# Kernel optimization log

Hardware: AMD Instinct MI355X
Metric: run time of the kernel (lower is better)

The kernel has to match this reference:

```python
import jax, jax.numpy as jnp
import numpy as np

K_NEIGHBORS = 8  # sparse_reads


def setup_inputs() -> dict:
    key = jax.random.key(0)
    k1, k2, k3, k4 = jax.random.split(key, 4)
    b, m, w, r, d_in = 32, 65536, 32, 4, 256
    xi = jax.random.normal(k1, (b, d_in), jnp.float32)
    sparse = jax.random.normal(k2, (b, m, w), jnp.float32)
    W_rk = jax.random.normal(k3, (r * w, d_in), jnp.float32) * 0.05  # read_keys_transform weight
    b_rk = jax.random.normal(k4, (r * w,), jnp.float32) * 0.01       # read_keys_transform bias
    return {"xi": xi, "sparse": sparse, "W_rk": W_rk, "b_rk": b_rk}


def reference(xi, sparse, W_rk, b_rk):
    b = xi.shape[0]
    m, w = sparse.shape[1], sparse.shape[2]
    r = W_rk.shape[0] // w
    # read keys: Linear(input_size, r*w) -> [b, r, w]
    read_keys = (xi @ W_rk.T + b_rk).reshape(b, r, w)
    # exact kNN replacing FLANN: squared L2 distances [b, r, m]
    d2 = (
        jnp.sum(read_keys * read_keys, -1)[..., None]
        - 2.0 * jnp.einsum('brw,bmw->brm', read_keys, sparse)
        + jnp.sum(sparse * sparse, -1)[:, None, :]
    )
    neg_d, idx = jax.lax.top_k(-d2, K_NEIGHBORS)  # K smallest distances
    dist = -neg_d                                  # [b, r, K]
    # gather the K nearest memory rows per (batch, head): [b, r, K, w]
    vecs = sparse[jnp.arange(b)[:, None, None], idx]
    # distances normalized by their max (per key), as in `distances / max(distances)`
    read_weights = dist / jnp.max(dist, -1, keepdims=True)
    # torch code stacks per-key over batch then over keys -> [r, b, K, w]
    read_vectors = jnp.transpose(vecs, (1, 0, 2, 3))
    read_weights = jnp.transpose(read_weights, (1, 0, 2))  # [r, b, K]
    return read_vectors, read_weights
```

## Files before the change

kernel.cpp:

```cpp
#include <hip/hip_runtime.h>

constexpr int Bb = 32;
constexpr int Mm = 65536;
constexpr int Ww = 32;
constexpr int Rr = 4;
constexpr int Dd = 256;
constexpr int Kk = 8;

constexpr int NB_A = 64;
constexpr int TPB_A = 256;
constexpr int ROWS_PER_BLOCK = Mm / NB_A;
constexpr int TILE_ROWS = 128;
constexpr int TILES = ROWS_PER_BLOCK / TILE_ROWS;
constexpr int NBUF = 3;
constexpr int GRP_F4 = 65;
constexpr int TILE_F4 = (TILE_ROWS / 8) * GRP_F4;
constexpr int CPL = NB_A * Kk / 64;

__device__ __forceinline__ void glds16(const float4* src, float4* dst_lds) {
  __builtin_amdgcn_global_load_lds(
      (const __attribute__((address_space(1))) void*)src,
      (__attribute__((address_space(3))) void*)dst_lds, 16, 0, 0);
}

__global__ __launch_bounds__(128) void rk_kernel(
    const float* __restrict__ xi, const float* __restrict__ Wrk,
    const float* __restrict__ brk, float* __restrict__ rk,
    float* __restrict__ rknorm) {
  const int b = blockIdx.x;
  const int tid = threadIdx.x;
  __shared__ float xs[Dd];
  __shared__ float rks[Rr * Ww];
  #pragma unroll
  for (int i = 0; i < Dd; i += 128) xs[i + tid] = xi[b * Dd + i + tid];
  __syncthreads();
  float acc = brk[tid];
  const float4* wr = reinterpret_cast<const float4*>(Wrk + (size_t)tid * Dd);
  #pragma unroll 4
  for (int i = 0; i < Dd / 4; ++i) {
    float4 wv = wr[i];
    acc = fmaf(wv.x, xs[4 * i + 0], acc);
    acc = fmaf(wv.y, xs[4 * i + 1], acc);
    acc = fmaf(wv.z, xs[4 * i + 2], acc);
    acc = fmaf(wv.w, xs[4 * i + 3], acc);
  }
  rk[b * Rr * Ww + tid] = acc;
  rks[tid] = acc;
  __syncthreads();
  if (tid < Rr) {
    float s = 0.f;
    #pragma unroll
    for (int j = 0; j < Ww; ++j) s = fmaf(rks[tid * Ww + j], rks[tid * Ww + j], s);
    rknorm[b * Rr + tid] = s;
  }
}

__global__ __launch_bounds__(TPB_A, 2) void topk_partial(
    const float* __restrict__ sparse, const float* __restrict__ rk,
    const float* __restrict__ rknorm, float* __restrict__ cand_d,
    int* __restrict__ cand_i) {
  const int b = blockIdx.y;
  const int tid = threadIdx.x;
  const int lane = tid & 63;
  const int wid = tid >> 6;
  const float INF = __builtin_inff();

  __shared__ float4 rk4[Rr][8];
  __shared__ float rkn_s[Rr];
  __shared__ float4 tile[NBUF][TILE_F4];

  if (tid < Rr * Ww) reinterpret_cast<float*>(rk4)[tid] = rk[b * Rr * Ww + tid];
  if (tid < Rr) rkn_s[tid] = rknorm[b * Rr + tid];
  __syncthreads();

  float rkn[Rr];
  #pragma unroll
  for (int r = 0; r < Rr; ++r) rkn[r] = rkn_s[r];

  const int rowBlk = blockIdx.x * ROWS_PER_BLOCK;
  const float4* sb4 =
      reinterpret_cast<const float4*>(sparse) + (size_t)b * Mm * 8;

  const int rowL = wid * 32 + (lane >> 1);
  const int hsel = (tid & 1) * 4;
  const int rbase = (rowL >> 3) * GRP_F4 + (rowL & 7) * 8;

  float d8[Rr][TILES];

  auto STAGE = [&](int buf, int t) {
    const float4* g0 = sb4 + (size_t)(rowBlk + t * TILE_ROWS + wid * 32) * 8;
    #pragma unroll
    for (int i = 0; i < 4; ++i)
      glds16(g0 + i * 64 + lane, &tile[buf][(wid * 4 + i) * GRP_F4]);
  };

  STAGE(0, 0);
  STAGE(1, 1);
  #pragma unroll
  for (int t = 0; t < TILES; ++t) {
    if (t + 2 < TILES) {
      asm volatile("s_waitcnt lgkmcnt(0)" ::: "memory");
      STAGE((t + 2) % NBUF, t + 2);
      asm volatile("s_waitcnt vmcnt(8)" ::: "memory");
    } else if (t + 1 < TILES) {
      asm volatile("s_waitcnt vmcnt(4)" ::: "memory");
    } else {
      asm volatile("s_waitcnt vmcnt(0)" ::: "memory");
    }
    const float4* tb = &tile[t % NBUF][rbase];
    float a0 = 0.f, a1 = 0.f, a2 = 0.f, a3 = 0.f, ss = 0.f;
    #pragma unroll
    for (int j = 0; j < 4; ++j) {
      float4 v = tb[hsel + j];
      float4 k0 = rk4[0][hsel + j];
      float4 k1 = rk4[1][hsel + j];
      float4 k2 = rk4[2][hsel + j];
      float4 k3 = rk4[3][hsel + j];
      a0 = fmaf(k0.x, v.x, a0); a0 = fmaf(k0.y, v.y, a0);
      a0 = fmaf(k0.z, v.z, a0); a0 = fmaf(k0.w, v.w, a0);
      a1 = fmaf(k1.x, v.x, a1); a1 = fmaf(k1.y, v.y, a1);
      a1 = fmaf(k1.z, v.z, a1); a1 = fmaf(k1.w, v.w, a1);
      a2 = fmaf(k2.x, v.x, a2); a2 = fmaf(k2.y, v.y, a2);
      a2 = fmaf(k2.z, v.z, a2); a2 = fmaf(k2.w, v.w, a2);
      a3 = fmaf(k3.x, v.x, a3); a3 = fmaf(k3.y, v.y, a3);
      a3 = fmaf(k3.z, v.z, a3); a3 = fmaf(k3.w, v.w, a3);
      ss = fmaf(v.x, v.x, ss); ss = fmaf(v.y, v.y, ss);
      ss = fmaf(v.z, v.z, ss); ss = fmaf(v.w, v.w, ss);
    }
    float p0 = fmaf(-2.f, a0, ss);
    float p1 = fmaf(-2.f, a1, ss);
    float p2 = fmaf(-2.f, a2, ss);
    float p3 = fmaf(-2.f, a3, ss);
    p0 += __shfl_xor(p0, 1);
    p1 += __shfl_xor(p1, 1);
    p2 += __shfl_xor(p2, 1);
    p3 += __shfl_xor(p3, 1);
    d8[0][t] = p0 + rkn[0];
    d8[1][t] = p1 + rkn[1];
    d8[2][t] = p2 + rkn[2];
    d8[3][t] = p3 + rkn[3];
  }

  __syncthreads();
  float* dmp = reinterpret_cast<float*>(&tile[0][0]);
  if ((tid & 1) == 0) {
    const int e = tid >> 1;
    #pragma unroll
    for (int r = 0; r < Rr; ++r) {
      float4* p = reinterpret_cast<float4*>(&dmp[(r * 128 + e) * 8]);
      p[0] = make_float4(d8[r][0], d8[r][1], d8[r][2], d8[r][3]);
      p[1] = make_float4(d8[r][4], d8[r][5], d8[r][6], d8[r][7]);
    }
  }
  __syncthreads();

  {
    const int r = wid;
    const int e0 = 2 * lane;
    float v[2][TILES];
    #pragma unroll
    for (int q = 0; q < 2; ++q) {
      const float4* p =
          reinterpret_cast<const float4*>(&dmp[(r * 128 + e0 + q) * 8]);
      float4 lo = p[0], hi = p[1];
      v[q][0] = lo.x; v[q][1] = lo.y; v[q][2] = lo.z; v[q][3] = lo.w;
      v[q][4] = hi.x; v[q][5] = hi.y; v[q][6] = hi.z; v[q][7] = hi.w;
    }
    const int base = rowBlk + e0;
    size_t o = ((size_t)(b * Rr + r) * NB_A + blockIdx.x) * Kk;
    #pragma unroll
    for (int k = 0; k < Kk; ++k) {
      float lv = v[0][0];
      int lrow = base;
      #pragma unroll
      for (int q = 0; q < 2; ++q)
        #pragma unroll
        for (int s = 0; s < TILES; ++s) {
          if (q == 0 && s == 0) continue;
          int row = base + q + s * TILE_ROWS;
          if (v[q][s] < lv || (v[q][s] == lv && row < lrow)) {
            lv = v[q][s]; lrow = row;
          }
        }
      float bv = lv;
      int bi = lrow;
      #pragma unroll
      for (int off = 32; off; off >>= 1) {
        float ov = __shfl_xor(bv, off);
        int oi = __shfl_xor(bi, off);
        if (ov < bv || (ov == bv && oi < bi)) { bv = ov; bi = oi; }
      }
      if (lane == 0) { cand_d[o + k] = bv; cand_i[o + k] = bi; }
      #pragma unroll
      for (int q = 0; q < 2; ++q)
        #pragma unroll
        for (int s = 0; s < TILES; ++s) {
          bool clr = (v[q][s] == bv) && (base + q + s * TILE_ROWS == bi);
          v[q][s] = clr ? INF : v[q][s];
        }
    }
  }
}

__global__ __launch_bounds__(64) void topk_final(
    const float* __restrict__ sparse, const float* __restrict__ cand_d,
    const int* __restrict__ cand_i, float* __restrict__ out) {
  const int br = blockIdx.x;
  const int b = br >> 2;
  const int r = br & 3;
  const int lane = threadIdx.x;
  const float INF = __builtin_inff();

  float ld[CPL];
  int li[CPL];
  const float* cd = cand_d + (size_t)br * (NB_A * Kk);
  const int* ci = cand_i + (size_t)br * (NB_A * Kk);
  #pragma unroll
  for (int t = 0; t < CPL; ++t) {
    ld[t] = cd[t * 64 + lane];
    li[t] = ci[t * 64 + lane];
  }
  #pragma unroll
  for (int i = 0; i < CPL - 1; ++i)
    #pragma unroll
    for (int j = 0; j < CPL - 1 - i; ++j)
      if (ld[j + 1] < ld[j] || (ld[j + 1] == ld[j] && li[j + 1] < li[j])) {
        float td = ld[j]; ld[j] = ld[j + 1]; ld[j + 1] = td;
        int ti = li[j]; li[j] = li[j + 1]; li[j + 1] = ti;
      }

  __shared__ float s_td[Kk];
  __shared__ int s_ti[Kk];
  #pragma unroll
  for (int k = 0; k < Kk; ++k) {
    float v = ld[0];
    int id = li[0];
    #pragma unroll
    for (int off = 32; off; off >>= 1) {
      float ov = __shfl_xor(v, off);
      int oi = __shfl_xor(id, off);
      if (ov < v || (ov == v && oi < id)) { v = ov; id = oi; }
    }
    if (lane == 0) { s_td[k] = v; s_ti[k] = id; }
    if (li[0] == id) {
      #pragma unroll
      for (int j = 0; j < CPL - 1; ++j) { ld[j] = ld[j + 1]; li[j] = li[j + 1]; }
      ld[CPL - 1] = INF;
      li[CPL - 1] = -1;
    }
  }
  __syncthreads();

  const float dmax = s_td[Kk - 1];
  if (lane < Kk)
    out[(size_t)Rr * Bb * Kk * Ww + ((size_t)r * Bb + b) * Kk + lane] =
        s_td[lane] / dmax;

  const float* sbase = sparse + (size_t)b * Mm * Ww;
  #pragma unroll
  for (int t = 0; t < (Kk * Ww) / 64; ++t) {
    int e = t * 64 + lane;
    int k = e >> 5;
    int j = e & 31;
    out[(((size_t)r * Bb + b) * Kk + k) * Ww + j] =
        sbase[(size_t)s_ti[k] * Ww + j];
  }
}

extern "C" void kernel_launch(void* const* d_in, const int* in_sizes, int n_in,
                              void* d_out, int out_size, void* d_ws,
                              size_t ws_size, hipStream_t stream) {
  const float* xi = (const float*)d_in[0];
  const float* sparse = (const float*)d_in[1];
  const float* Wrk = (const float*)d_in[2];
  const float* brk = (const float*)d_in[3];
  float* out = (float*)d_out;

  char* ws = (char*)d_ws;
  float* rk = (float*)ws;
  float* rknorm = (float*)(ws + 16384);
  float* cand_d = (float*)(ws + 16896);
  int* cand_i = (int*)(ws + 16896 + 262144);

  rk_kernel<<<Bb, 128, 0, stream>>>(xi, Wrk, brk, rk, rknorm);
  dim3 gridA(NB_A, Bb);
  topk_partial<<<gridA, TPB_A, 0, stream>>>(sparse, rk, rknorm, cand_d, cand_i);
  topk_final<<<Bb * Rr, 64, 0, stream>>>(sparse, cand_d, cand_i, out);
}
```

Measured before the change: 91.84 us.

## Replace LDS-staged async tile loads with register double-buffered direct global loads

```diff
diff --git a/kernel.cpp b/kernel.cpp
--- a/kernel.cpp
+++ b/kernel.cpp
@@ -12,16 +12,7 @@
 constexpr int ROWS_PER_BLOCK = Mm / NB_A;
 constexpr int TILE_ROWS = 128;
 constexpr int TILES = ROWS_PER_BLOCK / TILE_ROWS;
-constexpr int NBUF = 3;
-constexpr int GRP_F4 = 65;
-constexpr int TILE_F4 = (TILE_ROWS / 8) * GRP_F4;
 constexpr int CPL = NB_A * Kk / 64;
-
-__device__ __forceinline__ void glds16(const float4* src, float4* dst_lds) {
-  __builtin_amdgcn_global_load_lds(
-      (const __attribute__((address_space(1))) void*)src,
-      (__attribute__((address_space(3))) void*)dst_lds, 16, 0, 0);
-}
 
 __global__ __launch_bounds__(128) void rk_kernel(
     const float* __restrict__ xi, const float* __restrict__ Wrk,
@@ -67,7 +58,7 @@
 
   __shared__ float4 rk4[Rr][8];
   __shared__ float rkn_s[Rr];
-  __shared__ float4 tile[NBUF][TILE_F4];
+  __shared__ float dmp[Rr * TILE_ROWS * TILES];
 
   if (tid < Rr * Ww) reinterpret_cast<float*>(rk4)[tid] = rk[b * Rr * Ww + tid];
   if (tid < Rr) rkn_s[tid] = rknorm[b * Rr + tid];
@@ -78,40 +69,30 @@
   for (int r = 0; r < Rr; ++r) rkn[r] = rkn_s[r];
 
   const int rowBlk = blockIdx.x * ROWS_PER_BLOCK;
-  const float4* sb4 =
-      reinterpret_cast<const float4*>(sparse) + (size_t)b * Mm * 8;
-
   const int rowL = wid * 32 + (lane >> 1);
   const int hsel = (tid & 1) * 4;
-  const int rbase = (rowL >> 3) * GRP_F4 + (rowL & 7) * 8;
+
+  const float4* rp = reinterpret_cast<const float4*>(sparse) +
+                     (size_t)b * Mm * 8 + (size_t)(rowBlk + rowL) * 8 + hsel;
 
   float d8[Rr][TILES];
 
-  auto STAGE = [&](int buf, int t) {
-    const float4* g0 = sb4 + (size_t)(rowBlk + t * TILE_ROWS + wid * 32) * 8;
-    #pragma unroll
-    for (int i = 0; i < 4; ++i)
-      glds16(g0 + i * 64 + lane, &tile[buf][(wid * 4 + i) * GRP_F4]);
-  };
-
-  STAGE(0, 0);
-  STAGE(1, 1);
+  float4 La0, La1, La2, La3, Lb0, Lb1, Lb2, Lb3;
+  La0 = rp[0]; La1 = rp[1]; La2 = rp[2]; La3 = rp[3];
   #pragma unroll
   for (int t = 0; t < TILES; ++t) {
-    if (t + 2 < TILES) {
-      asm volatile("s_waitcnt lgkmcnt(0)" ::: "memory");
-      STAGE((t + 2) % NBUF, t + 2);
-      asm volatile("s_waitcnt vmcnt(8)" ::: "memory");
-    } else if (t + 1 < TILES) {
-      asm volatile("s_waitcnt vmcnt(4)" ::: "memory");
-    } else {
-      asm volatile("s_waitcnt vmcnt(0)" ::: "memory");
-    }
-    const float4* tb = &tile[t % NBUF][rbase];
+    const float4* np = rp + (size_t)(t + 1) * TILE_ROWS * 8;
+    float4 v0, v1, v2, v3;
+    if (t & 1) { v0 = Lb0; v1 = Lb1; v2 = Lb2; v3 = Lb3; }
+    else       { v0 = La0; v1 = La1; v2 = La2; v3 = La3; }
+    if (t + 1 < TILES) {
+      if (t & 1) { La0 = np[0]; La1 = np[1]; La2 = np[2]; La3 = np[3]; }
+      else       { Lb0 = np[0]; Lb1 = np[1]; Lb2 = np[2]; Lb3 = np[3]; }
+    }
     float a0 = 0.f, a1 = 0.f, a2 = 0.f, a3 = 0.f, ss = 0.f;
     #pragma unroll
     for (int j = 0; j < 4; ++j) {
-      float4 v = tb[hsel + j];
+      float4 v = (j == 0) ? v0 : (j == 1) ? v1 : (j == 2) ? v2 : v3;
       float4 k0 = rk4[0][hsel + j];
       float4 k1 = rk4[1][hsel + j];
       float4 k2 = rk4[2][hsel + j];
@@ -142,7 +123,6 @@
   }
 
   __syncthreads();
-  float* dmp = reinterpret_cast<float*>(&tile[0][0]);
   if ((tid & 1) == 0) {
     const int e = tid >> 1;
     #pragma unroll
```

Measured after the change: 95.80 us. 4.3% more time.

## Fuse read-key projection and final top-k merge into single partial top-k kernel

Applied to the files above, without the earlier changes.

```diff
diff --git a/kernel.cpp b/kernel.cpp
--- a/kernel.cpp
+++ b/kernel.cpp
@@ -23,54 +23,53 @@
       (__attribute__((address_space(3))) void*)dst_lds, 16, 0, 0);
 }
 
-__global__ __launch_bounds__(128) void rk_kernel(
-    const float* __restrict__ xi, const float* __restrict__ Wrk,
-    const float* __restrict__ brk, float* __restrict__ rk,
-    float* __restrict__ rknorm) {
-  const int b = blockIdx.x;
-  const int tid = threadIdx.x;
-  __shared__ float xs[Dd];
-  __shared__ float rks[Rr * Ww];
-  #pragma unroll
-  for (int i = 0; i < Dd; i += 128) xs[i + tid] = xi[b * Dd + i + tid];
-  __syncthreads();
-  float acc = brk[tid];
-  const float4* wr = reinterpret_cast<const float4*>(Wrk + (size_t)tid * Dd);
-  #pragma unroll 4
-  for (int i = 0; i < Dd / 4; ++i) {
-    float4 wv = wr[i];
-    acc = fmaf(wv.x, xs[4 * i + 0], acc);
-    acc = fmaf(wv.y, xs[4 * i + 1], acc);
-    acc = fmaf(wv.z, xs[4 * i + 2], acc);
-    acc = fmaf(wv.w, xs[4 * i + 3], acc);
-  }
-  rk[b * Rr * Ww + tid] = acc;
-  rks[tid] = acc;
-  __syncthreads();
-  if (tid < Rr) {
-    float s = 0.f;
-    #pragma unroll
-    for (int j = 0; j < Ww; ++j) s = fmaf(rks[tid * Ww + j], rks[tid * Ww + j], s);
-    rknorm[b * Rr + tid] = s;
-  }
-}
-
-__global__ __launch_bounds__(TPB_A, 2) void topk_partial(
-    const float* __restrict__ sparse, const float* __restrict__ rk,
-    const float* __restrict__ rknorm, float* __restrict__ cand_d,
-    int* __restrict__ cand_i) {
+__global__ __launch_bounds__(TPB_A, 2) void topk_fused(
+    const float* __restrict__ xi, const float* __restrict__ sparse,
+    const float* __restrict__ Wrk, const float* __restrict__ brk,
+    float* __restrict__ cand_d, int* __restrict__ cand_i,
+    int* __restrict__ cnt, float* __restrict__ out) {
   const int b = blockIdx.y;
   const int tid = threadIdx.x;
   const int lane = tid & 63;
   const int wid = tid >> 6;
   const float INF = __builtin_inff();
 
+  __shared__ float xs[Dd];
   __shared__ float4 rk4[Rr][8];
   __shared__ float rkn_s[Rr];
   __shared__ float4 tile[NBUF][TILE_F4];
-
-  if (tid < Rr * Ww) reinterpret_cast<float*>(rk4)[tid] = rk[b * Rr * Ww + tid];
-  if (tid < Rr) rkn_s[tid] = rknorm[b * Rr + tid];
+  __shared__ float s_td[4][Kk];
+  __shared__ int s_ti[4][Kk];
+  __shared__ int lastFlag;
+
+  if (tid < Dd / 4)
+    reinterpret_cast<float4*>(xs)[tid] =
+        reinterpret_cast<const float4*>(xi + (size_t)b * Dd)[tid];
+  __syncthreads();
+  {
+    const int i = tid >> 1;
+    const int h = tid & 1;
+    const float4* wr =
+        reinterpret_cast<const float4*>(Wrk) + (size_t)i * 64 + h * 32;
+    const float4* xv = reinterpret_cast<const float4*>(xs) + h * 32;
+    float acc = 0.f;
+    #pragma unroll 8
+    for (int j = 0; j < 32; ++j) {
+      float4 w = wr[j], x = xv[j];
+      acc = fmaf(w.x, x.x, acc); acc = fmaf(w.y, x.y, acc);
+      acc = fmaf(w.z, x.z, acc); acc = fmaf(w.w, x.w, acc);
+    }
+    acc += __shfl_xor(acc, 1);
+    if (h == 0) reinterpret_cast<float*>(rk4)[i] = acc + brk[i];
+  }
+  __syncthreads();
+  if (tid < Rr) {
+    const float* p = reinterpret_cast<const float*>(rk4) + tid * 32;
+    float s = 0.f;
+    #pragma unroll
+    for (int j = 0; j < Ww; ++j) s = fmaf(p[j], p[j], s);
+    rkn_s[tid] = s;
+  }
   __syncthreads();
 
   float rkn[Rr];
@@ -190,7 +189,12 @@
         int oi = __shfl_xor(bi, off);
         if (ov < bv || (ov == bv && oi < bi)) { bv = ov; bi = oi; }
       }
-      if (lane == 0) { cand_d[o + k] = bv; cand_i[o + k] = bi; }
+      if (lane == 0) {
+        __hip_atomic_store(&cand_d[o + k], bv, __ATOMIC_RELAXED,
+                           __HIP_MEMORY_SCOPE_AGENT);
+        __hip_atomic_store(&cand_i[o + k], bi, __ATOMIC_RELAXED,
+                           __HIP_MEMORY_SCOPE_AGENT);
+      }
       #pragma unroll
       for (int q = 0; q < 2; ++q)
         #pragma unroll
@@ -200,70 +204,70 @@
         }
     }
   }
-}
-
-__global__ __launch_bounds__(64) void topk_final(
-    const float* __restrict__ sparse, const float* __restrict__ cand_d,
-    const int* __restrict__ cand_i, float* __restrict__ out) {
-  const int br = blockIdx.x;
-  const int b = br >> 2;
-  const int r = br & 3;
-  const int lane = threadIdx.x;
-  const float INF = __builtin_inff();
-
-  float ld[CPL];
-  int li[CPL];
-  const float* cd = cand_d + (size_t)br * (NB_A * Kk);
-  const int* ci = cand_i + (size_t)br * (NB_A * Kk);
-  #pragma unroll
-  for (int t = 0; t < CPL; ++t) {
-    ld[t] = cd[t * 64 + lane];
-    li[t] = ci[t * 64 + lane];
-  }
-  #pragma unroll
-  for (int i = 0; i < CPL - 1; ++i)
-    #pragma unroll
-    for (int j = 0; j < CPL - 1 - i; ++j)
-      if (ld[j + 1] < ld[j] || (ld[j + 1] == ld[j] && li[j + 1] < li[j])) {
-        float td = ld[j]; ld[j] = ld[j + 1]; ld[j + 1] = td;
-        int ti = li[j]; li[j] = li[j + 1]; li[j + 1] = ti;
-      }
-
-  __shared__ float s_td[Kk];
-  __shared__ int s_ti[Kk];
-  #pragma unroll
-  for (int k = 0; k < Kk; ++k) {
-    float v = ld[0];
-    int id = li[0];
-    #pragma unroll
-    for (int off = 32; off; off >>= 1) {
-      float ov = __shfl_xor(v, off);
-      int oi = __shfl_xor(id, off);
-      if (ov < v || (ov == v && oi < id)) { v = ov; id = oi; }
-    }
-    if (lane == 0) { s_td[k] = v; s_ti[k] = id; }
-    if (li[0] == id) {
-      #pragma unroll
-      for (int j = 0; j < CPL - 1; ++j) { ld[j] = ld[j + 1]; li[j] = li[j + 1]; }
-      ld[CPL - 1] = INF;
-      li[CPL - 1] = -1;
-    }
-  }
-  __syncthreads();
-
-  const float dmax = s_td[Kk - 1];
-  if (lane < Kk)
-    out[(size_t)Rr * Bb * Kk * Ww + ((size_t)r * Bb + b) * Kk + lane] =
-        s_td[lane] / dmax;
-
-  const float* sbase = sparse + (size_t)b * Mm * Ww;
-  #pragma unroll
-  for (int t = 0; t < (Kk * Ww) / 64; ++t) {
-    int e = t * 64 + lane;
-    int k = e >> 5;
-    int j = e & 31;
-    out[(((size_t)r * Bb + b) * Kk + k) * Ww + j] =
-        sbase[(size_t)s_ti[k] * Ww + j];
+
+  __syncthreads();
+  if (tid == 0) {
+    __threadfence();
+    int prev = __hip_atomic_fetch_add(&cnt[b], 1, __ATOMIC_ACQ_REL,
+                                      __HIP_MEMORY_SCOPE_AGENT);
+    lastFlag = (prev == NB_A - 1);
+  }
+  __syncthreads();
+  if (!lastFlag) return;
+  __threadfence();
+
+  {
+    const int r = wid;
+    const float* cd = cand_d + (size_t)(b * Rr + r) * (NB_A * Kk);
+    const int* ci = cand_i + (size_t)(b * Rr + r) * (NB_A * Kk);
+    float ld[CPL];
+    int li[CPL];
+    #pragma unroll
+    for (int t = 0; t < CPL; ++t) {
+      ld[t] = __hip_atomic_load(&cd[t * 64 + lane], __ATOMIC_RELAXED,
+                                __HIP_MEMORY_SCOPE_AGENT);
+      li[t] = __hip_atomic_load(&ci[t * 64 + lane], __ATOMIC_RELAXED,
+                                __HIP_MEMORY_SCOPE_AGENT);
+    }
+    #pragma unroll
+    for (int i = 0; i < CPL - 1; ++i)
+      #pragma unroll
+      for (int j = 0; j < CPL - 1 - i; ++j)
+        if (ld[j + 1] < ld[j] || (ld[j + 1] == ld[j] && li[j + 1] < li[j])) {
+          float td = ld[j]; ld[j] = ld[j + 1]; ld[j + 1] = td;
+          int ti = li[j]; li[j] = li[j + 1]; li[j + 1] = ti;
+        }
+    #pragma unroll
+    for (int k = 0; k < Kk; ++k) {
+      float mv = ld[0];
+      int mi = li[0];
+      #pragma unroll
+      for (int off = 32; off; off >>= 1) {
+        float ov = __shfl_xor(mv, off);
+        int oi = __shfl_xor(mi, off);
+        if (ov < mv || (ov == mv && oi < mi)) { mv = ov; mi = oi; }
+      }
+      if (lane == 0) { s_td[wid][k] = mv; s_ti[wid][k] = mi; }
+      if (li[0] == mi && ld[0] == mv) {
+        #pragma unroll
+        for (int j = 0; j < CPL - 1; ++j) { ld[j] = ld[j + 1]; li[j] = li[j + 1]; }
+        ld[CPL - 1] = INF;
+        li[CPL - 1] = -1;
+      }
+    }
+    const float dmax = s_td[wid][Kk - 1];
+    if (lane < Kk)
+      out[(size_t)Rr * Bb * Kk * Ww + ((size_t)r * Bb + b) * Kk + lane] =
+          s_td[wid][lane] / dmax;
+    const float* sbase = sparse + (size_t)b * Mm * Ww;
+    #pragma unroll
+    for (int t = 0; t < (Kk * Ww) / 64; ++t) {
+      int e = t * 64 + lane;
+      int k = e >> 5;
+      int j = e & 31;
+      out[(((size_t)r * Bb + b) * Kk + k) * Ww + j] =
+          sbase[(size_t)s_ti[wid][k] * Ww + j];
+    }
   }
 }
 
@@ -277,13 +281,12 @@
   float* out = (float*)d_out;
 
   char* ws = (char*)d_ws;
-  float* rk = (float*)ws;
-  float* rknorm = (float*)(ws + 16384);
-  float* cand_d = (float*)(ws + 16896);
-  int* cand_i = (int*)(ws + 16896 + 262144);
-
-  rk_kernel<<<Bb, 128, 0, stream>>>(xi, Wrk, brk, rk, rknorm);
-  dim3 gridA(NB_A, Bb);
-  topk_partial<<<gridA, TPB_A, 0, stream>>>(sparse, rk, rknorm, cand_d, cand_i);
-  topk_final<<<Bb * Rr, 64, 0, stream>>>(sparse, cand_d, cand_i, out);
+  float* cand_d = (float*)ws;
+  int* cand_i = (int*)(ws + 262144);
+  int* cnt = (int*)(ws + 524288);
+
+  hipMemsetAsync(cnt, 0, Bb * sizeof(int), stream);
+  dim3 grid(NB_A, Bb);
+  topk_fused<<<grid, TPB_A, 0, stream>>>(xi, sparse, Wrk, brk,
+                                         cand_d, cand_i, cnt, out);
 }
```

New measurement: 180.1 us. +96.1%, slower.
